# Kernel tuning notes

Measured on AMD Instinct MI355X. Metric: run time of the kernel, lower is better.

The kernel has to match this reference:

```python
import jax, jax.numpy as jnp
import numpy as np

N_WORD, N_TOPIC, N_DOC = 50000, 2000, 50000
D_WORD, D_TOPIC, D_OUT = 256, 128, 128
E_WW, E_WT, E_WD, E_TD, E_TT = 500000, 400000, 500000, 400000, 300000


def setup_inputs() -> dict:
    key = jax.random.key(0)
    ks = jax.random.split(key, 32)
    i = iter(range(32))

    def randn(shape, scale=1.0):
        return jax.random.normal(ks[next(i)], shape, dtype=jnp.float32) * scale

    def edges(n_e, n_src, n_dst):
        src = jax.random.randint(ks[next(i)], (n_e,), 0, n_src, dtype=jnp.int32)
        dst = jax.random.randint(ks[next(i)], (n_e,), 0, n_dst, dtype=jnp.int32)
        w = jax.random.uniform(ks[next(i)], (n_e,), dtype=jnp.float32)
        return src, dst, w

    feat_word = randn((N_WORD, D_WORD))
    feat_topic = randn((N_TOPIC, D_TOPIC))
    ww_src, ww_dst, ww_w = edges(E_WW, N_WORD, N_WORD)
    wt_src, wt_dst, wt_w = edges(E_WT, N_WORD, N_TOPIC)
    wd_src, wd_dst, wd_w = edges(E_WD, N_WORD, N_DOC)
    td_src, td_dst, td_w = edges(E_TD, N_TOPIC, N_DOC)
    tt_src, tt_dst, tt_w = edges(E_TT, N_TOPIC, N_TOPIC)
    return dict(
        feat_word=feat_word, feat_topic=feat_topic,
        ww_src=ww_src, ww_dst=ww_dst, ww_w=ww_w,
        wt_src=wt_src, wt_dst=wt_dst, wt_w=wt_w,
        wd_src=wd_src, wd_dst=wd_dst, wd_w=wd_w,
        td_src=td_src, td_dst=td_dst, td_w=td_w,
        tt_src=tt_src, tt_dst=tt_dst, tt_w=tt_w,
        W_ww=randn((D_WORD, D_OUT), 0.02), b_ww=randn((D_OUT,), 0.02),
        W_wt=randn((D_WORD, D_OUT), 0.02), b_wt=randn((D_OUT,), 0.02),
        W_wd=randn((D_WORD, D_OUT), 0.02), b_wd=randn((D_OUT,), 0.02),
        W_td=randn((D_TOPIC, D_OUT), 0.02), b_td=randn((D_OUT,), 0.02),
        W_tt=randn((D_TOPIC, D_OUT), 0.02), b_tt=randn((D_OUT,), 0.02),
    )


def _mean_agg(Wh, src, dst, w, n_dst):
    # u_mul_e: gather src feature, scale by edge weight; fn.mean: divide by in-degree
    m = Wh[src] * w[:, None]                                   # [E, D_OUT]
    s = jax.ops.segment_sum(m, dst, num_segments=n_dst)        # [n_dst, D_OUT]
    deg = jax.ops.segment_sum(jnp.ones_like(w), dst, num_segments=n_dst)
    return jnp.where(deg[:, None] > 0, s / jnp.maximum(deg, 1.0)[:, None], 0.0)


def reference(feat_word, feat_topic,
              ww_src, ww_dst, ww_w, wt_src, wt_dst, wt_w,
              wd_src, wd_dst, wd_w, td_src, td_dst, td_w,
              tt_src, tt_dst, tt_w,
              W_ww, b_ww, W_wt, b_wt, W_wd, b_wd, W_td, b_td, W_tt, b_tt):
    # Per-relation projections (note: in the torch source the causal/noise
    # branches are overwritten by the plain Linear, so this is the effective math).
    Wh_ww = feat_word @ W_ww + b_ww
    Wh_wt = feat_word @ W_wt + b_wt
    Wh_wd = feat_word @ W_wd + b_wd
    Wh_td = feat_topic @ W_td + b_td
    Wh_tt = feat_topic @ W_tt + b_tt
    # mean per edge type, then cross-etype 'sum' per destination node type
    h_word = _mean_agg(Wh_ww, ww_src, ww_dst, ww_w, N_WORD)
    h_topic = (_mean_agg(Wh_wt, wt_src, wt_dst, wt_w, N_TOPIC)
               + _mean_agg(Wh_tt, tt_src, tt_dst, tt_w, N_TOPIC))
    h_doc = (_mean_agg(Wh_wd, wd_src, wd_dst, wd_w, N_DOC)
             + _mean_agg(Wh_td, td_src, td_dst, td_w, N_DOC))
    return h_word, h_topic, h_doc
```

## Files before the change

kernel.cpp:

```cpp
#include <hip/hip_runtime.h>

typedef short short8 __attribute__((ext_vector_type(8)));
typedef float floatx4 __attribute__((ext_vector_type(4)));

__device__ __forceinline__ float b2f(unsigned int u16) {
    union { unsigned int i; float f; } v;
    v.i = u16 << 16;
    return v.f;
}
__device__ __forceinline__ unsigned short f2b(float f) {
    unsigned int i = __float_as_uint(f);
    unsigned int r = (i + 0x7FFFu + ((i >> 16) & 1u)) >> 16;
    return (unsigned short)r;
}

#define N_WORD  50000
#define N_TOPIC 2000
#define N_DOC   50000
#define CHAIN_END 0xFFFFFFFFu
#define NB_GEMM 814
#define NSLOT_WW (N_WORD * 8)
#define NSLOT_WT (N_TOPIC * 4)
#define NSLOT_TT (N_TOPIC * 4)
#define NSLOT_WD (N_DOC * 4)
#define NSLOT_TD (N_DOC * 4)
#define NSLOT_ALL (NSLOT_WW + NSLOT_WT + NSLOT_TT + NSLOT_WD + NSLOT_TD)

__global__ void detect_kernel(const unsigned int* __restrict__ feat_u32,
                              unsigned int* __restrict__ flag)
{
    int cnt = 0;
    for (int i = 0; i < 256; ++i) {
        unsigned int u = feat_u32[i];
        int e = (u >> 7) & 0xFF;
        if (e >= 110 && e <= 140) ++cnt;
    }
    *flag = (cnt > 128) ? 1u : 0u;
}

__global__ __launch_bounds__(256) void swizzle_kernel(
    const void* __restrict__ W0, const void* __restrict__ W1,
    const void* __restrict__ W2, const void* __restrict__ W3,
    const void* __restrict__ W4,
    const void* __restrict__ b0, const void* __restrict__ b1,
    const void* __restrict__ b2, const void* __restrict__ b3,
    const void* __restrict__ b4,
    short8* __restrict__ D0, short8* __restrict__ D1,
    short8* __restrict__ D2, short8* __restrict__ D3,
    short8* __restrict__ D4,
    unsigned short* __restrict__ bias_out,
    const unsigned int* __restrict__ flag_p)
{
    const int w = blockIdx.y;
    const void* W; const void* bs; short8* D; int S;
    switch (w) {
        case 0: W = W0; bs = b0; D = D0; S = 8; break;
        case 1: W = W1; bs = b1; D = D1; S = 8; break;
        case 2: W = W2; bs = b2; D = D2; S = 8; break;
        case 3: W = W3; bs = b3; D = D3; S = 4; break;
        default: W = W4; bs = b4; D = D4; S = 4; break;
    }
    const int n_entries = S * 8 * 64;
    const int mode = (int)*flag_p;
    for (int e = blockIdx.x * 256 + threadIdx.x; e < n_entries; e += 8 * 256) {
        const int lane = e & 63, t = (e >> 6) & 7, s = e >> 9;
        const int q = lane >> 4, n = t * 16 + (lane & 15);
        short8 val;
#pragma unroll
        for (int j = 0; j < 8; ++j) {
            const int k = s * 32 + q * 8 + j;
            unsigned short hv = mode ? ((const unsigned short*)W)[k * 128 + n]
                                     : f2b(((const float*)W)[k * 128 + n]);
            val[j] = (short)hv;
        }
        D[e] = val;
    }
    if (blockIdx.x == 0 && threadIdx.x < 128) {
        bias_out[w * 128 + threadIdx.x] =
            mode ? ((const unsigned short*)bs)[threadIdx.x]
                 : f2b(((const float*)bs)[threadIdx.x]);
    }
}

template <int S, int NP>
__device__ __forceinline__ void gemm_body_lds(
    short8* __restrict__ Blds,
    const void* feat_, int n_rows, int bx,
    const short8* Ba, const short8* Bb, const short8* Bc,
    const unsigned short* bias_all, int ba, int bb, int bc,
    unsigned short* Oa, unsigned short* Ob, unsigned short* Oc,
    int mode_bf16)
{
    const int tid = threadIdx.x;
    const int lane = tid & 63;
    const int wave = tid >> 6;
    const int row0 = (bx * 4 + wave) * 16;
    const int m = lane & 15, q = lane >> 4;
    const int K = S * 32;
    int arow_idx = row0 + m;
    if (arow_idx >= n_rows) arow_idx = n_rows - 1;

    short8 a[S];
    if (mode_bf16) {
        const short8* arow = (const short8*)((const unsigned short*)feat_ + (size_t)arow_idx * K);
#pragma unroll
        for (int s = 0; s < S; ++s) a[s] = arow[s * 4 + q];
    } else {
        const float* arow = (const float*)feat_ + (size_t)arow_idx * K;
#pragma unroll
        for (int s = 0; s < S; ++s) {
            const float4 f0 = ((const float4*)arow)[s * 8 + q * 2];
            const float4 f1 = ((const float4*)arow)[s * 8 + q * 2 + 1];
            short8 t;
            t[0] = (short)f2b(f0.x); t[1] = (short)f2b(f0.y);
            t[2] = (short)f2b(f0.z); t[3] = (short)f2b(f0.w);
            t[4] = (short)f2b(f1.x); t[5] = (short)f2b(f1.y);
            t[6] = (short)f2b(f1.z); t[7] = (short)f2b(f1.w);
            a[s] = t;
        }
    }

    constexpr int NH = (S * 8 * 64 > 2048) ? 2 : 1;
    constexpr int SH = S / NH;

#pragma unroll
    for (int p = 0; p < NP; ++p) {
        const short8* B = (p == 0) ? Ba : ((p == 1) ? Bb : Bc);
        const unsigned short* bias = bias_all + ((p == 0) ? ba : ((p == 1) ? bb : bc)) * 128;
        unsigned short* O = (p == 0) ? Oa : ((p == 1) ? Ob : Oc);

        floatx4 acc[8];
#pragma unroll
        for (int t = 0; t < 8; ++t) { acc[t][0] = 0.f; acc[t][1] = 0.f; acc[t][2] = 0.f; acc[t][3] = 0.f; }

#pragma unroll
        for (int h = 0; h < NH; ++h) {
            __syncthreads();
            for (int i = tid; i < SH * 8 * 64; i += 256) Blds[i] = B[h * (SH * 8 * 64) + i];
            __syncthreads();
#pragma unroll
            for (int s = 0; s < SH; ++s) {
#pragma unroll
                for (int t = 0; t < 8; ++t) {
                    short8 b = Blds[(s * 8 + t) * 64 + lane];
                    acc[t] = __builtin_amdgcn_mfma_f32_16x16x32_bf16(a[h * SH + s], b, acc[t], 0, 0, 0);
                }
            }
        }

#pragma unroll
        for (int t = 0; t < 8; ++t) {
            const float bb_ = b2f((unsigned int)bias[t * 16 + m]);
#pragma unroll
            for (int r = 0; r < 4; ++r) {
                const int row = row0 + q * 4 + r;
                if (row < n_rows)
                    O[(size_t)row * 128 + t * 16 + m] = f2b(acc[t][r] + bb_);
            }
        }
    }
}

__global__ __launch_bounds__(256) void link_gemm_kernel(
    const void* __restrict__ feat_word, const void* __restrict__ feat_topic,
    const short8* __restrict__ Bww, const short8* __restrict__ Bwt,
    const short8* __restrict__ Bwd, const short8* __restrict__ Btt,
    const short8* __restrict__ Btd,
    const unsigned short* __restrict__ bias_all,
    unsigned short* __restrict__ Wh_ww, unsigned short* __restrict__ Wh_wt,
    unsigned short* __restrict__ Wh_wd, unsigned short* __restrict__ Wh_tt,
    unsigned short* __restrict__ Wh_td,
    const int* s0, const int* d0, const void* w0, int n0, unsigned int* h0, unsigned long long* e0,
    const int* s1, const int* d1, const void* w1, int n1, unsigned int* h1, unsigned long long* e1,
    const int* s2, const int* d2, const void* w2, int n2, unsigned int* h2, unsigned long long* e2,
    const int* s3, const int* d3, const void* w3, int n3, unsigned int* h3, unsigned long long* e3,
    const int* s4, const int* d4, const void* w4, int n4, unsigned int* h4, unsigned long long* e4,
    const unsigned int* __restrict__ flag_p)
{
    __shared__ short8 Blds[2048];
    const int mode = (int)*flag_p;

    if (blockIdx.x < NB_GEMM) {
        if (blockIdx.x < 782) {
            gemm_body_lds<8, 3>(Blds, feat_word, N_WORD, blockIdx.x, Bww, Bwt, Bwd,
                                bias_all, 0, 1, 2, Wh_ww, Wh_wt, Wh_wd, mode);
        } else {
            gemm_body_lds<4, 2>(Blds, feat_topic, N_TOPIC, blockIdx.x - 782, Btt, Btd,
                                (const short8*)nullptr, bias_all, 4, 3, 0,
                                Wh_tt, Wh_td, (unsigned short*)nullptr, mode);
        }
        return;
    }

    int lb = blockIdx.x - NB_GEMM;
    const int nb0 = (n0 + 255) >> 8, nb1 = (n1 + 255) >> 8, nb2 = (n2 + 255) >> 8,
              nb3 = (n3 + 255) >> 8;
    const int* src; const int* dst; const void* w_; int n;
    unsigned int* head; unsigned long long* ent; int H;
    if (lb < nb0)      { src = s0; dst = d0; w_ = w0; n = n0; head = h0; ent = e0; H = 8; }
    else if ((lb -= nb0) < nb1) { src = s1; dst = d1; w_ = w1; n = n1; head = h1; ent = e1; H = 4; }
    else if ((lb -= nb1) < nb2) { src = s2; dst = d2; w_ = w2; n = n2; head = h2; ent = e2; H = 4; }
    else if ((lb -= nb2) < nb3) { src = s3; dst = d3; w_ = w3; n = n3; head = h3; ent = e3; H = 4; }
    else { lb -= nb3;  src = s4; dst = d4; w_ = w4; n = n4; head = h4; ent = e4; H = 4; }

    const int i = lb * 256 + threadIdx.x;
    if (i >= n) return;
    const int d = dst[i];
    const unsigned int slot = (unsigned int)d * H + ((unsigned int)i & (H - 1));
    const unsigned int old = atomicExch(&head[slot], (unsigned int)i);
    const unsigned short w16 = mode ? ((const unsigned short*)w_)[i]
                                    : f2b(((const float*)w_)[i]);
    ent[i] = ((unsigned long long)old << 32)
           | ((unsigned long long)w16 << 16)
           | (unsigned long long)(unsigned int)src[i];
}

__device__ __forceinline__ void acc8(float a[8], const uint4& u, float w)
{
    a[0] += b2f(u.x & 0xffffu) * w; a[1] += b2f(u.x >> 16) * w;
    a[2] += b2f(u.y & 0xffffu) * w; a[3] += b2f(u.y >> 16) * w;
    a[4] += b2f(u.z & 0xffffu) * w; a[5] += b2f(u.z >> 16) * w;
    a[6] += b2f(u.w & 0xffffu) * w; a[7] += b2f(u.w >> 16) * w;
}
__device__ __forceinline__ uint4 rowld(const unsigned short* Wh, unsigned int pay, int sl)
{
    return ((const uint4*)(Wh + (size_t)(pay & 0xffffu) * 128))[sl];
}

__device__ __forceinline__ void walk2s(
    const unsigned long long* __restrict__ ent, const unsigned short* __restrict__ Wh,
    unsigned int e1, unsigned int e2, int sl, float a[8], float& cnt)
{
    bool l1 = (e1 != CHAIN_END), l2 = (e2 != CHAIN_END);
    unsigned long long v1 = 0, v2 = 0;
    if (l1) v1 = ent[e1];
    if (l2) v2 = ent[e2];
    while (l1 || l2) {
        const unsigned int n1 = (unsigned int)(v1 >> 32);
        const unsigned int n2 = (unsigned int)(v2 >> 32);
        const bool l1n = l1 && (n1 != CHAIN_END);
        const bool l2n = l2 && (n2 != CHAIN_END);
        unsigned long long v1n = 0, v2n = 0;
        if (l1n) v1n = ent[n1];
        if (l2n) v2n = ent[n2];
        uint4 u1, u2;
        if (l1) u1 = rowld(Wh, (unsigned int)v1, sl);
        if (l2) u2 = rowld(Wh, (unsigned int)v2, sl);
        if (l1) { acc8(a, u1, b2f(((unsigned int)v1) >> 16)); cnt += 1.0f; }
        if (l2) { acc8(a, u2, b2f(((unsigned int)v2) >> 16)); cnt += 1.0f; }
        v1 = v1n; v2 = v2n; l1 = l1n; l2 = l2n;
    }
}

__device__ __forceinline__ void walk2(
    const unsigned long long* __restrict__ ent1, const unsigned short* __restrict__ Wh1, unsigned int e1,
    const unsigned long long* __restrict__ ent2, const unsigned short* __restrict__ Wh2, unsigned int e2,
    int sl, float a1[8], float a2[8], float& c1, float& c2)
{
    bool l1 = (e1 != CHAIN_END), l2 = (e2 != CHAIN_END);
    unsigned long long v1 = 0, v2 = 0;
    if (l1) v1 = ent1[e1];
    if (l2) v2 = ent2[e2];
    while (l1 || l2) {
        const unsigned int n1 = (unsigned int)(v1 >> 32);
        const unsigned int n2 = (unsigned int)(v2 >> 32);
        const bool l1n = l1 && (n1 != CHAIN_END);
        const bool l2n = l2 && (n2 != CHAIN_END);
        unsigned long long v1n = 0, v2n = 0;
        if (l1n) v1n = ent1[n1];
        if (l2n) v2n = ent2[n2];
        uint4 u1, u2;
        if (l1) u1 = rowld(Wh1, (unsigned int)v1, sl);
        if (l2) u2 = rowld(Wh2, (unsigned int)v2, sl);
        if (l1) { acc8(a1, u1, b2f(((unsigned int)v1) >> 16)); c1 += 1.0f; }
        if (l2) { acc8(a2, u2, b2f(((unsigned int)v2) >> 16)); c2 += 1.0f; }
        v1 = v1n; v2 = v2n; l1 = l1n; l2 = l2n;
    }
}

__device__ __forceinline__ void write8(
    void* out, size_t off_elems, int node, int sl, const float r[8], int mode)
{
    if (mode) {
        uint4 o;
        o.x = (unsigned int)f2b(r[0]) | ((unsigned int)f2b(r[1]) << 16);
        o.y = (unsigned int)f2b(r[2]) | ((unsigned int)f2b(r[3]) << 16);
        o.z = (unsigned int)f2b(r[4]) | ((unsigned int)f2b(r[5]) << 16);
        o.w = (unsigned int)f2b(r[6]) | ((unsigned int)f2b(r[7]) << 16);
        *(uint4*)((unsigned short*)out + off_elems + (size_t)node * 128 + sl * 8) = o;
    } else {
        float* p = (float*)out + off_elems + (size_t)node * 128 + sl * 8;
        ((float4*)p)[0] = make_float4(r[0], r[1], r[2], r[3]);
        ((float4*)p)[1] = make_float4(r[4], r[5], r[6], r[7]);
    }
}

__global__ __launch_bounds__(256) void gather_topic_kernel(
    const unsigned int* __restrict__ h_wt, const unsigned long long* __restrict__ e_wt,
    const unsigned short* __restrict__ Wh_wt,
    const unsigned int* __restrict__ h_tt, const unsigned long long* __restrict__ e_tt,
    const unsigned short* __restrict__ Wh_tt,
    void* __restrict__ out,
    const unsigned int* __restrict__ flag_p)
{
    const int mode = (int)*flag_p;
    const int sl = threadIdx.x & 15;
    const int grp = (threadIdx.x >> 4) & 3;
    const int wave = threadIdx.x >> 6;
    const int node = blockIdx.x * 4 + wave;
    float a1[8] = {0,0,0,0,0,0,0,0}, a2[8] = {0,0,0,0,0,0,0,0};
    float c1 = 0.f, c2 = 0.f;
    walk2(e_wt, Wh_wt, h_wt[node * 4 + grp], e_tt, Wh_tt, h_tt[node * 4 + grp],
          sl, a1, a2, c1, c2);
#pragma unroll
    for (int j = 0; j < 8; ++j) {
        a1[j] += __shfl_xor(a1[j], 16); a1[j] += __shfl_xor(a1[j], 32);
        a2[j] += __shfl_xor(a2[j], 16); a2[j] += __shfl_xor(a2[j], 32);
    }
    c1 += __shfl_xor(c1, 16); c1 += __shfl_xor(c1, 32);
    c2 += __shfl_xor(c2, 16); c2 += __shfl_xor(c2, 32);
    const float i1 = (c1 > 0.f) ? 1.f / c1 : 0.f;
    const float i2 = (c2 > 0.f) ? 1.f / c2 : 0.f;
    float r[8];
#pragma unroll
    for (int j = 0; j < 8; ++j) r[j] = a1[j] * i1 + a2[j] * i2;
    if (grp == 0) write8(out, (size_t)6400000, node, sl, r, mode);
}

__global__ __launch_bounds__(256) void gather_dw_kernel(
    const unsigned int* __restrict__ h_wd, const unsigned long long* __restrict__ e_wd,
    const unsigned short* __restrict__ Wh_wd,
    const unsigned int* __restrict__ h_td, const unsigned long long* __restrict__ e_td,
    const unsigned short* __restrict__ Wh_td,
    const unsigned int* __restrict__ h_ww, const unsigned long long* __restrict__ e_ww,
    const unsigned short* __restrict__ Wh_ww,
    void* __restrict__ out,
    const unsigned int* __restrict__ flag_p)
{
    const int mode = (int)*flag_p;
    const int sl = threadIdx.x & 15;
    const int grp = (threadIdx.x >> 4) & 3;
    const int wave = threadIdx.x >> 6;

    if (blockIdx.x < 12500) {
        const int node = blockIdx.x * 4 + wave;
        float a1[8] = {0,0,0,0,0,0,0,0}, a2[8] = {0,0,0,0,0,0,0,0};
        float c1 = 0.f, c2 = 0.f;
        walk2(e_wd, Wh_wd, h_wd[node * 4 + grp], e_td, Wh_td, h_td[node * 4 + grp],
              sl, a1, a2, c1, c2);
#pragma unroll
        for (int j = 0; j < 8; ++j) {
            a1[j] += __shfl_xor(a1[j], 16); a1[j] += __shfl_xor(a1[j], 32);
            a2[j] += __shfl_xor(a2[j], 16); a2[j] += __shfl_xor(a2[j], 32);
        }
        c1 += __shfl_xor(c1, 16); c1 += __shfl_xor(c1, 32);
        c2 += __shfl_xor(c2, 16); c2 += __shfl_xor(c2, 32);
        const float i1 = (c1 > 0.f) ? 1.f / c1 : 0.f;
        const float i2 = (c2 > 0.f) ? 1.f / c2 : 0.f;
        float r[8];
#pragma unroll
        for (int j = 0; j < 8; ++j) r[j] = a1[j] * i1 + a2[j] * i2;
        if (grp == 0) write8(out, (size_t)6656000, node, sl, r, mode);
    } else {
        const int node = (blockIdx.x - 12500) * 4 + wave;
        float a[8] = {0,0,0,0,0,0,0,0}; float cnt = 0.f;
        walk2s(e_ww, Wh_ww, h_ww[node * 8 + grp * 2], h_ww[node * 8 + grp * 2 + 1],
               sl, a, cnt);
#pragma unroll
        for (int j = 0; j < 8; ++j) { a[j] += __shfl_xor(a[j], 16); a[j] += __shfl_xor(a[j], 32); }
        cnt += __shfl_xor(cnt, 16); cnt += __shfl_xor(cnt, 32);
        const float inv = (cnt > 0.f) ? 1.f / cnt : 0.f;
        float r[8];
#pragma unroll
        for (int j = 0; j < 8; ++j) r[j] = a[j] * inv;
        if (grp == 0) write8(out, 0, node, sl, r, mode);
    }
}

extern "C" void kernel_launch(void* const* d_in, const int* in_sizes, int n_in,
                              void* d_out, int out_size, void* d_ws, size_t ws_size,
                              hipStream_t stream)
{
    const void* feat_word  = d_in[0];
    const void* feat_topic = d_in[1];
    const int* ww_src = (const int*)d_in[2];
    const int* ww_dst = (const int*)d_in[3];
    const void* ww_w = d_in[4];
    const int* wt_src = (const int*)d_in[5];
    const int* wt_dst = (const int*)d_in[6];
    const void* wt_w = d_in[7];
    const int* wd_src = (const int*)d_in[8];
    const int* wd_dst = (const int*)d_in[9];
    const void* wd_w = d_in[10];
    const int* td_src = (const int*)d_in[11];
    const int* td_dst = (const int*)d_in[12];
    const void* td_w = d_in[13];
    const int* tt_src = (const int*)d_in[14];
    const int* tt_dst = (const int*)d_in[15];
    const void* tt_w = d_in[16];
    const void* W_ww = d_in[17];
    const void* b_ww = d_in[18];
    const void* W_wt = d_in[19];
    const void* b_wt = d_in[20];
    const void* W_wd = d_in[21];
    const void* b_wd = d_in[22];
    const void* W_td = d_in[23];
    const void* b_td = d_in[24];
    const void* W_tt = d_in[25];
    const void* b_tt = d_in[26];

    const int E_ww = in_sizes[2];
    const int E_wt = in_sizes[5];
    const int E_wd = in_sizes[8];
    const int E_td = in_sizes[11];
    const int E_tt = in_sizes[14];

    char* ws = (char*)d_ws;
    unsigned int* flag = (unsigned int*)ws;
    unsigned int* head_base = (unsigned int*)(ws + 16);
    unsigned int* h_ww = head_base;
    unsigned int* h_wt = h_ww + NSLOT_WW;
    unsigned int* h_tt = h_wt + NSLOT_WT;
    unsigned int* h_wd = h_tt + NSLOT_TT;
    unsigned int* h_td = h_wd + NSLOT_WD;
    size_t off = 16 + (size_t)NSLOT_ALL * 4;
    off = (off + 15) & ~(size_t)15;
    short8* Bsw_ww = (short8*)(ws + off); off += 65536;
    short8* Bsw_wt = (short8*)(ws + off); off += 65536;
    short8* Bsw_wd = (short8*)(ws + off); off += 65536;
    short8* Bsw_td = (short8*)(ws + off); off += 32768;
    short8* Bsw_tt = (short8*)(ws + off); off += 32768;
    unsigned short* bias_all = (unsigned short*)(ws + off); off += 5 * 128 * 2;
    off = (off + 15) & ~(size_t)15;
    unsigned short* Wh_ww = (unsigned short*)(ws + off); off += (size_t)N_WORD * 128 * 2;
    unsigned short* Wh_wd = (unsigned short*)(ws + off); off += (size_t)N_WORD * 128 * 2;
    unsigned short* Wh_tt = (unsigned short*)(ws + off); off += (size_t)N_TOPIC * 128 * 2;
    unsigned short* Wh_td = (unsigned short*)(ws + off); off += (size_t)N_TOPIC * 128 * 2;
    off = (off + 7) & ~(size_t)7;
    unsigned long long* e_ww = (unsigned long long*)(ws + off); off += (size_t)E_ww * 8;
    unsigned long long* e_wt = (unsigned long long*)(ws + off); off += (size_t)E_wt * 8;
    unsigned long long* e_tt = (unsigned long long*)(ws + off); off += (size_t)E_tt * 8;
    unsigned long long* e_wd = (unsigned long long*)(ws + off); off += (size_t)E_wd * 8;
    unsigned long long* e_td = (unsigned long long*)(ws + off); off += (size_t)E_td * 8;

    unsigned short* Wh_wt = (unsigned short*)d_out;

    detect_kernel<<<1, 1, 0, stream>>>((const unsigned int*)feat_word, flag);
    hipMemsetAsync(head_base, 0xFF, (size_t)NSLOT_ALL * 4, stream);

    swizzle_kernel<<<dim3(8, 5), 256, 0, stream>>>(
        W_ww, W_wt, W_wd, W_td, W_tt, b_ww, b_wt, b_wd, b_td, b_tt,
        Bsw_ww, Bsw_wt, Bsw_wd, Bsw_td, Bsw_tt, bias_all, flag);

    const int nb_link = ((E_ww + 255) / 256) + ((E_wt + 255) / 256) +
                        ((E_tt + 255) / 256) + ((E_wd + 255) / 256) +
                        ((E_td + 255) / 256);
    link_gemm_kernel<<<NB_GEMM + nb_link, 256, 0, stream>>>(
        feat_word, feat_topic, Bsw_ww, Bsw_wt, Bsw_wd, Bsw_tt, Bsw_td,
        bias_all, Wh_ww, Wh_wt, Wh_wd, Wh_tt, Wh_td,
        ww_src, ww_dst, ww_w, E_ww, h_ww, e_ww,
        wt_src, wt_dst, wt_w, E_wt, h_wt, e_wt,
        tt_src, tt_dst, tt_w, E_tt, h_tt, e_tt,
        wd_src, wd_dst, wd_w, E_wd, h_wd, e_wd,
        td_src, td_dst, td_w, E_td, h_td, e_td, flag);

    gather_topic_kernel<<<500, 256, 0, stream>>>(
        h_wt, e_wt, Wh_wt, h_tt, e_tt, Wh_tt, d_out, flag);

    gather_dw_kernel<<<25000, 256, 0, stream>>>(
        h_wd, e_wd, Wh_wd, h_td, e_td, Wh_td,
        h_ww, e_ww, Wh_ww, d_out, flag);
}
```

Before: 402.9 us.

## Store first edge payload in 64-bit chain heads and regroup gather kernels

Each head slot becomes a 64-bit value holding the newest edge's payload plus the next index, swapped in with a 64-bit atomicExch. The entry array now stores the displaced head, so the first hop of every chain needs no dependent load. The word-word relation drops from 8 to 4 chains per node. The topic and doc gathers are merged into one launch and word-word gets its own, with Wh_wd moved into the output buffer as scratch. The cost is twice the head memset bytes, 64-bit atomics, and longer chains for word-word.

```diff
diff --git a/kernel.cpp b/kernel.cpp
--- a/kernel.cpp
+++ b/kernel.cpp
@@ -17,9 +17,10 @@
 #define N_WORD  50000
 #define N_TOPIC 2000
 #define N_DOC   50000
-#define CHAIN_END 0xFFFFFFFFu
+#define CHAIN_END   0xFFFFFFFFu
+#define PAY_INVALID 0xFFFFFFFFu
 #define NB_GEMM 814
-#define NSLOT_WW (N_WORD * 8)
+#define NSLOT_WW (N_WORD * 4)
 #define NSLOT_WT (N_TOPIC * 4)
 #define NSLOT_TT (N_TOPIC * 4)
 #define NSLOT_WD (N_DOC * 4)
@@ -170,11 +171,11 @@
     unsigned short* __restrict__ Wh_ww, unsigned short* __restrict__ Wh_wt,
     unsigned short* __restrict__ Wh_wd, unsigned short* __restrict__ Wh_tt,
     unsigned short* __restrict__ Wh_td,
-    const int* s0, const int* d0, const void* w0, int n0, unsigned int* h0, unsigned long long* e0,
-    const int* s1, const int* d1, const void* w1, int n1, unsigned int* h1, unsigned long long* e1,
-    const int* s2, const int* d2, const void* w2, int n2, unsigned int* h2, unsigned long long* e2,
-    const int* s3, const int* d3, const void* w3, int n3, unsigned int* h3, unsigned long long* e3,
-    const int* s4, const int* d4, const void* w4, int n4, unsigned int* h4, unsigned long long* e4,
+    const int* s0, const int* d0, const void* w0, int n0, unsigned long long* h0, unsigned long long* e0,
+    const int* s1, const int* d1, const void* w1, int n1, unsigned long long* h1, unsigned long long* e1,
+    const int* s2, const int* d2, const void* w2, int n2, unsigned long long* h2, unsigned long long* e2,
+    const int* s3, const int* d3, const void* w3, int n3, unsigned long long* h3, unsigned long long* e3,
+    const int* s4, const int* d4, const void* w4, int n4, unsigned long long* h4, unsigned long long* e4,
     const unsigned int* __restrict__ flag_p)
 {
     __shared__ short8 Blds[2048];
@@ -196,23 +197,24 @@
     const int nb0 = (n0 + 255) >> 8, nb1 = (n1 + 255) >> 8, nb2 = (n2 + 255) >> 8,
               nb3 = (n3 + 255) >> 8;
     const int* src; const int* dst; const void* w_; int n;
-    unsigned int* head; unsigned long long* ent; int H;
-    if (lb < nb0)      { src = s0; dst = d0; w_ = w0; n = n0; head = h0; ent = e0; H = 8; }
-    else if ((lb -= nb0) < nb1) { src = s1; dst = d1; w_ = w1; n = n1; head = h1; ent = e1; H = 4; }
-    else if ((lb -= nb1) < nb2) { src = s2; dst = d2; w_ = w2; n = n2; head = h2; ent = e2; H = 4; }
-    else if ((lb -= nb2) < nb3) { src = s3; dst = d3; w_ = w3; n = n3; head = h3; ent = e3; H = 4; }
-    else { lb -= nb3;  src = s4; dst = d4; w_ = w4; n = n4; head = h4; ent = e4; H = 4; }
+    unsigned long long* head8; unsigned long long* ent;
+    if (lb < nb0)      { src = s0; dst = d0; w_ = w0; n = n0; head8 = h0; ent = e0; }
+    else if ((lb -= nb0) < nb1) { src = s1; dst = d1; w_ = w1; n = n1; head8 = h1; ent = e1; }
+    else if ((lb -= nb1) < nb2) { src = s2; dst = d2; w_ = w2; n = n2; head8 = h2; ent = e2; }
+    else if ((lb -= nb2) < nb3) { src = s3; dst = d3; w_ = w3; n = n3; head8 = h3; ent = e3; }
+    else { lb -= nb3;  src = s4; dst = d4; w_ = w4; n = n4; head8 = h4; ent = e4; }
 
     const int i = lb * 256 + threadIdx.x;
     if (i >= n) return;
     const int d = dst[i];
-    const unsigned int slot = (unsigned int)d * H + ((unsigned int)i & (H - 1));
-    const unsigned int old = atomicExch(&head[slot], (unsigned int)i);
     const unsigned short w16 = mode ? ((const unsigned short*)w_)[i]
                                     : f2b(((const float*)w_)[i]);
-    ent[i] = ((unsigned long long)old << 32)
-           | ((unsigned long long)w16 << 16)
-           | (unsigned long long)(unsigned int)src[i];
+    const unsigned int pay = ((unsigned int)w16 << 16) | (unsigned int)src[i];
+    const unsigned long long X = ((unsigned long long)(unsigned int)i << 32)
+                               | (unsigned long long)pay;
+    const unsigned int slot = (unsigned int)d * 4 + ((unsigned int)i & 3);
+    const unsigned long long old8 = atomicExch(&head8[slot], X);
+    ent[i] = old8;
 }
 
 __device__ __forceinline__ void acc8(float a[8], const uint4& u, float w)
@@ -227,40 +229,34 @@
     return ((const uint4*)(Wh + (size_t)(pay & 0xffffu) * 128))[sl];
 }
 
-__device__ __forceinline__ void walk2s(
+__device__ __forceinline__ void walk1e(
     const unsigned long long* __restrict__ ent, const unsigned short* __restrict__ Wh,
-    unsigned int e1, unsigned int e2, int sl, float a[8], float& cnt)
-{
-    bool l1 = (e1 != CHAIN_END), l2 = (e2 != CHAIN_END);
-    unsigned long long v1 = 0, v2 = 0;
-    if (l1) v1 = ent[e1];
-    if (l2) v2 = ent[e2];
-    while (l1 || l2) {
-        const unsigned int n1 = (unsigned int)(v1 >> 32);
-        const unsigned int n2 = (unsigned int)(v2 >> 32);
-        const bool l1n = l1 && (n1 != CHAIN_END);
-        const bool l2n = l2 && (n2 != CHAIN_END);
-        unsigned long long v1n = 0, v2n = 0;
-        if (l1n) v1n = ent[n1];
-        if (l2n) v2n = ent[n2];
-        uint4 u1, u2;
-        if (l1) u1 = rowld(Wh, (unsigned int)v1, sl);
-        if (l2) u2 = rowld(Wh, (unsigned int)v2, sl);
-        if (l1) { acc8(a, u1, b2f(((unsigned int)v1) >> 16)); cnt += 1.0f; }
-        if (l2) { acc8(a, u2, b2f(((unsigned int)v2) >> 16)); cnt += 1.0f; }
-        v1 = v1n; v2 = v2n; l1 = l1n; l2 = l2n;
-    }
-}
-
-__device__ __forceinline__ void walk2(
-    const unsigned long long* __restrict__ ent1, const unsigned short* __restrict__ Wh1, unsigned int e1,
-    const unsigned long long* __restrict__ ent2, const unsigned short* __restrict__ Wh2, unsigned int e2,
+    unsigned long long v, int sl, float a[8], float& cnt)
+{
+    while (true) {
+        const unsigned int nx = (unsigned int)(v >> 32);
+        const bool ln = (nx != CHAIN_END);
+        unsigned long long vn = 0;
+        if (ln) vn = ent[nx];
+        const unsigned int pay = (unsigned int)v;
+        if (pay != PAY_INVALID) {
+            const uint4 u = rowld(Wh, pay, sl);
+            acc8(a, u, b2f(pay >> 16));
+            cnt += 1.0f;
+        }
+        if (!ln) break;
+        v = vn;
+    }
+}
+
+__device__ __forceinline__ void walk2e(
+    const unsigned long long* __restrict__ ent1, const unsigned short* __restrict__ Wh1,
+    unsigned long long v1,
+    const unsigned long long* __restrict__ ent2, const unsigned short* __restrict__ Wh2,
+    unsigned long long v2,
     int sl, float a1[8], float a2[8], float& c1, float& c2)
 {
-    bool l1 = (e1 != CHAIN_END), l2 = (e2 != CHAIN_END);
-    unsigned long long v1 = 0, v2 = 0;
-    if (l1) v1 = ent1[e1];
-    if (l2) v2 = ent2[e2];
+    bool l1 = true, l2 = true;
     while (l1 || l2) {
         const unsigned int n1 = (unsigned int)(v1 >> 32);
         const unsigned int n2 = (unsigned int)(v2 >> 32);
@@ -269,11 +265,15 @@
         unsigned long long v1n = 0, v2n = 0;
         if (l1n) v1n = ent1[n1];
         if (l2n) v2n = ent2[n2];
+        const unsigned int p1 = (unsigned int)v1;
+        const unsigned int p2 = (unsigned int)v2;
+        const bool d1 = l1 && (p1 != PAY_INVALID);
+        const bool d2 = l2 && (p2 != PAY_INVALID);
         uint4 u1, u2;
-        if (l1) u1 = rowld(Wh1, (unsigned int)v1, sl);
-        if (l2) u2 = rowld(Wh2, (unsigned int)v2, sl);
-        if (l1) { acc8(a1, u1, b2f(((unsigned int)v1) >> 16)); c1 += 1.0f; }
-        if (l2) { acc8(a2, u2, b2f(((unsigned int)v2) >> 16)); c2 += 1.0f; }
+        if (d1) u1 = rowld(Wh1, p1, sl);
+        if (d2) u2 = rowld(Wh2, p2, sl);
+        if (d1) { acc8(a1, u1, b2f(p1 >> 16)); c1 += 1.0f; }
+        if (d2) { acc8(a2, u2, b2f(p2 >> 16)); c2 += 1.0f; }
         v1 = v1n; v2 = v2n; l1 = l1n; l2 = l2n;
     }
 }
@@ -295,11 +295,61 @@
     }
 }
 
-__global__ __launch_bounds__(256) void gather_topic_kernel(
-    const unsigned int* __restrict__ h_wt, const unsigned long long* __restrict__ e_wt,
+__device__ __forceinline__ void dual_body(
+    const unsigned long long* __restrict__ h1, const unsigned long long* __restrict__ e1t,
+    const unsigned short* __restrict__ Wh1,
+    const unsigned long long* __restrict__ h2, const unsigned long long* __restrict__ e2t,
+    const unsigned short* __restrict__ Wh2,
+    void* __restrict__ out, size_t off_elems, int blk, int mode)
+{
+    const int sl = threadIdx.x & 15;
+    const int grp = (threadIdx.x >> 4) & 3;
+    const int wave = threadIdx.x >> 6;
+    const int node = blk * 4 + wave;
+    float a1[8] = {0,0,0,0,0,0,0,0}, a2[8] = {0,0,0,0,0,0,0,0};
+    float c1 = 0.f, c2 = 0.f;
+    walk2e(e1t, Wh1, h1[node * 4 + grp], e2t, Wh2, h2[node * 4 + grp],
+           sl, a1, a2, c1, c2);
+#pragma unroll
+    for (int j = 0; j < 8; ++j) {
+        a1[j] += __shfl_xor(a1[j], 16); a1[j] += __shfl_xor(a1[j], 32);
+        a2[j] += __shfl_xor(a2[j], 16); a2[j] += __shfl_xor(a2[j], 32);
+    }
+    c1 += __shfl_xor(c1, 16); c1 += __shfl_xor(c1, 32);
+    c2 += __shfl_xor(c2, 16); c2 += __shfl_xor(c2, 32);
+    const float i1 = (c1 > 0.f) ? 1.f / c1 : 0.f;
+    const float i2 = (c2 > 0.f) ? 1.f / c2 : 0.f;
+    float r[8];
+#pragma unroll
+    for (int j = 0; j < 8; ++j) r[j] = a1[j] * i1 + a2[j] * i2;
+    if (grp == 0) write8(out, off_elems, node, sl, r, mode);
+}
+
+__global__ __launch_bounds__(256) void gather_dt_kernel(
+    const unsigned long long* __restrict__ h_wt, const unsigned long long* __restrict__ e_wt,
     const unsigned short* __restrict__ Wh_wt,
-    const unsigned int* __restrict__ h_tt, const unsigned long long* __restrict__ e_tt,
+    const unsigned long long* __restrict__ h_tt, const unsigned long long* __restrict__ e_tt,
     const unsigned short* __restrict__ Wh_tt,
+    const unsigned long long* __restrict__ h_wd, const unsigned long long* __restrict__ e_wd,
+    const unsigned short* __restrict__ Wh_wd,
+    const unsigned long long* __restrict__ h_td, const unsigned long long* __restrict__ e_td,
+    const unsigned short* __restrict__ Wh_td,
+    void* __restrict__ out,
+    const unsigned int* __restrict__ flag_p)
+{
+    const int mode = (int)*flag_p;
+    if (blockIdx.x < 500) {
+        dual_body(h_wt, e_wt, Wh_wt, h_tt, e_tt, Wh_tt,
+                  out, (size_t)6400000, blockIdx.x, mode);
+    } else {
+        dual_body(h_wd, e_wd, Wh_wd, h_td, e_td, Wh_td,
+                  out, (size_t)6656000, blockIdx.x - 500, mode);
+    }
+}
+
+__global__ __launch_bounds__(256) void gather_w_kernel(
+    const unsigned long long* __restrict__ h_ww, const unsigned long long* __restrict__ e_ww,
+    const unsigned short* __restrict__ Wh_ww,
     void* __restrict__ out,
     const unsigned int* __restrict__ flag_p)
 {
@@ -308,73 +358,16 @@
     const int grp = (threadIdx.x >> 4) & 3;
     const int wave = threadIdx.x >> 6;
     const int node = blockIdx.x * 4 + wave;
-    float a1[8] = {0,0,0,0,0,0,0,0}, a2[8] = {0,0,0,0,0,0,0,0};
-    float c1 = 0.f, c2 = 0.f;
-    walk2(e_wt, Wh_wt, h_wt[node * 4 + grp], e_tt, Wh_tt, h_tt[node * 4 + grp],
-          sl, a1, a2, c1, c2);
-#pragma unroll
-    for (int j = 0; j < 8; ++j) {
-        a1[j] += __shfl_xor(a1[j], 16); a1[j] += __shfl_xor(a1[j], 32);
-        a2[j] += __shfl_xor(a2[j], 16); a2[j] += __shfl_xor(a2[j], 32);
-    }
-    c1 += __shfl_xor(c1, 16); c1 += __shfl_xor(c1, 32);
-    c2 += __shfl_xor(c2, 16); c2 += __shfl_xor(c2, 32);
-    const float i1 = (c1 > 0.f) ? 1.f / c1 : 0.f;
-    const float i2 = (c2 > 0.f) ? 1.f / c2 : 0.f;
+    float a[8] = {0,0,0,0,0,0,0,0}; float cnt = 0.f;
+    walk1e(e_ww, Wh_ww, h_ww[node * 4 + grp], sl, a, cnt);
+#pragma unroll
+    for (int j = 0; j < 8; ++j) { a[j] += __shfl_xor(a[j], 16); a[j] += __shfl_xor(a[j], 32); }
+    cnt += __shfl_xor(cnt, 16); cnt += __shfl_xor(cnt, 32);
+    const float inv = (cnt > 0.f) ? 1.f / cnt : 0.f;
     float r[8];
 #pragma unroll
-    for (int j = 0; j < 8; ++j) r[j] = a1[j] * i1 + a2[j] * i2;
-    if (grp == 0) write8(out, (size_t)6400000, node, sl, r, mode);
-}
-
-__global__ __launch_bounds__(256) void gather_dw_kernel(
-    const unsigned int* __restrict__ h_wd, const unsigned long long* __restrict__ e_wd,
-    const unsigned short* __restrict__ Wh_wd,
-    const unsigned int* __restrict__ h_td, const unsigned long long* __restrict__ e_td,
-    const unsigned short* __restrict__ Wh_td,
-    const unsigned int* __restrict__ h_ww, const unsigned long long* __restrict__ e_ww,
-    const unsigned short* __restrict__ Wh_ww,
-    void* __restrict__ out,
-    const unsigned int* __restrict__ flag_p)
-{
-    const int mode = (int)*flag_p;
-    const int sl = threadIdx.x & 15;
-    const int grp = (threadIdx.x >> 4) & 3;
-    const int wave = threadIdx.x >> 6;
-
-    if (blockIdx.x < 12500) {
-        const int node = blockIdx.x * 4 + wave;
-        float a1[8] = {0,0,0,0,0,0,0,0}, a2[8] = {0,0,0,0,0,0,0,0};
-        float c1 = 0.f, c2 = 0.f;
-        walk2(e_wd, Wh_wd, h_wd[node * 4 + grp], e_td, Wh_td, h_td[node * 4 + grp],
-              sl, a1, a2, c1, c2);
-#pragma unroll
-        for (int j = 0; j < 8; ++j) {
-            a1[j] += __shfl_xor(a1[j], 16); a1[j] += __shfl_xor(a1[j], 32);
-            a2[j] += __shfl_xor(a2[j], 16); a2[j] += __shfl_xor(a2[j], 32);
-        }
-        c1 += __shfl_xor(c1, 16); c1 += __shfl_xor(c1, 32);
-        c2 += __shfl_xor(c2, 16); c2 += __shfl_xor(c2, 32);
-        const float i1 = (c1 > 0.f) ? 1.f / c1 : 0.f;
-        const float i2 = (c2 > 0.f) ? 1.f / c2 : 0.f;
-        float r[8];
-#pragma unroll
-        for (int j = 0; j < 8; ++j) r[j] = a1[j] * i1 + a2[j] * i2;
-        if (grp == 0) write8(out, (size_t)6656000, node, sl, r, mode);
-    } else {
-        const int node = (blockIdx.x - 12500) * 4 + wave;
-        float a[8] = {0,0,0,0,0,0,0,0}; float cnt = 0.f;
-        walk2s(e_ww, Wh_ww, h_ww[node * 8 + grp * 2], h_ww[node * 8 + grp * 2 + 1],
-               sl, a, cnt);
-#pragma unroll
-        for (int j = 0; j < 8; ++j) { a[j] += __shfl_xor(a[j], 16); a[j] += __shfl_xor(a[j], 32); }
-        cnt += __shfl_xor(cnt, 16); cnt += __shfl_xor(cnt, 32);
-        const float inv = (cnt > 0.f) ? 1.f / cnt : 0.f;
-        float r[8];
-#pragma unroll
-        for (int j = 0; j < 8; ++j) r[j] = a[j] * inv;
-        if (grp == 0) write8(out, 0, node, sl, r, mode);
-    }
+    for (int j = 0; j < 8; ++j) r[j] = a[j] * inv;
+    if (grp == 0) write8(out, 0, node, sl, r, mode);
 }
 
 extern "C" void kernel_launch(void* const* d_in, const int* in_sizes, int n_in,
@@ -417,13 +410,13 @@
 
     char* ws = (char*)d_ws;
     unsigned int* flag = (unsigned int*)ws;
-    unsigned int* head_base = (unsigned int*)(ws + 16);
-    unsigned int* h_ww = head_base;
-    unsigned int* h_wt = h_ww + NSLOT_WW;
-    unsigned int* h_tt = h_wt + NSLOT_WT;
-    unsigned int* h_wd = h_tt + NSLOT_TT;
-    unsigned int* h_td = h_wd + NSLOT_WD;
-    size_t off = 16 + (size_t)NSLOT_ALL * 4;
+    size_t off = 16;
+    unsigned long long* h_ww = (unsigned long long*)(ws + off);
+    unsigned long long* h_wt = h_ww + NSLOT_WW;
+    unsigned long long* h_tt = h_wt + NSLOT_WT;
+    unsigned long long* h_wd = h_tt + NSLOT_TT;
+    unsigned long long* h_td = h_wd + NSLOT_WD;
+    off += (size_t)NSLOT_ALL * 8;
     off = (off + 15) & ~(size_t)15;
     short8* Bsw_ww = (short8*)(ws + off); off += 65536;
     short8* Bsw_wt = (short8*)(ws + off); off += 65536;
@@ -433,7 +426,7 @@
     unsigned short* bias_all = (unsigned short*)(ws + off); off += 5 * 128 * 2;
     off = (off + 15) & ~(size_t)15;
     unsigned short* Wh_ww = (unsigned short*)(ws + off); off += (size_t)N_WORD * 128 * 2;
-    unsigned short* Wh_wd = (unsigned short*)(ws + off); off += (size_t)N_WORD * 128 * 2;
+    unsigned short* Wh_wt = (unsigned short*)(ws + off); off += (size_t)N_WORD * 128 * 2;
     unsigned short* Wh_tt = (unsigned short*)(ws + off); off += (size_t)N_TOPIC * 128 * 2;
     unsigned short* Wh_td = (unsigned short*)(ws + off); off += (size_t)N_TOPIC * 128 * 2;
     off = (off + 7) & ~(size_t)7;
@@ -443,10 +436,10 @@
     unsigned long long* e_wd = (unsigned long long*)(ws + off); off += (size_t)E_wd * 8;
     unsigned long long* e_td = (unsigned long long*)(ws + off); off += (size_t)E_td * 8;
 
-    unsigned short* Wh_wt = (unsigned short*)d_out;
+    unsigned short* Wh_wd = (unsigned short*)d_out;
 
     detect_kernel<<<1, 1, 0, stream>>>((const unsigned int*)feat_word, flag);
-    hipMemsetAsync(head_base, 0xFF, (size_t)NSLOT_ALL * 4, stream);
+    hipMemsetAsync(h_ww, 0xFF, (size_t)NSLOT_ALL * 8, stream);
 
     swizzle_kernel<<<dim3(8, 5), 256, 0, stream>>>(
         W_ww, W_wt, W_wd, W_td, W_tt, b_ww, b_wt, b_wd, b_td, b_tt,
@@ -464,10 +457,10 @@
         wd_src, wd_dst, wd_w, E_wd, h_wd, e_wd,
         td_src, td_dst, td_w, E_td, h_td, e_td, flag);
 
-    gather_topic_kernel<<<500, 256, 0, stream>>>(
-        h_wt, e_wt, Wh_wt, h_tt, e_tt, Wh_tt, d_out, flag);
-
-    gather_dw_kernel<<<25000, 256, 0, stream>>>(
-        h_wd, e_wd, Wh_wd, h_td, e_td, Wh_td,
+    gather_dt_kernel<<<500 + 12500, 256, 0, stream>>>(
+        h_wt, e_wt, Wh_wt, h_tt, e_tt, Wh_tt,
+        h_wd, e_wd, Wh_wd, h_td, e_td, Wh_td, d_out, flag);
+
+    gather_w_kernel<<<12500, 256, 0, stream>>>(
         h_ww, e_ww, Wh_ww, d_out, flag);
 }
```

Result: faster. 390.2 us (-3.2%).
